# Optimization experiments

Hardware: AMD Instinct MI355X
Metric: run time of the kernel (lower is better)

The kernel has to match this reference:

```python
import jax, jax.numpy as jnp
import numpy as np

V, T, E, H, L, B = 50257, 1024, 1024, 16, 12, 4
HD = E // H
FF = 4 * E
EPS = 1e-5


def layer_norm(x, g, b):
    m = jnp.mean(x, axis=-1, keepdims=True)
    v = jnp.mean((x - m) ** 2, axis=-1, keepdims=True)
    return (x - m) * jax.lax.rsqrt(v + EPS) * g + b


def setup_inputs() -> dict:
    key = jax.random.key(0)
    ks = jax.random.split(key, 24)
    s = 0.02
    inp = {
        'idx': jax.random.randint(ks[0], (B, T), 0, V),
        'targets': jax.random.randint(ks[1], (B, T), 0, V),
        'tok_emb': jax.random.normal(ks[2], (V, E), jnp.float32) * s,
        'pos_emb': jax.random.normal(ks[3], (T, E), jnp.float32) * s,
        'Wq': jax.random.normal(ks[4], (L, E, H, HD), jnp.float32) * s,
        'Wk': jax.random.normal(ks[5], (L, E, H, HD), jnp.float32) * s,
        'Wv': jax.random.normal(ks[6], (L, E, H, HD), jnp.float32) * s,
        'Wo': jax.random.normal(ks[7], (L, E, E), jnp.float32) * s,
        'bo': jnp.zeros((L, E), jnp.float32),
        'ln1_g': jnp.ones((L, E), jnp.float32),
        'ln1_b': jnp.zeros((L, E), jnp.float32),
        'ln2_g': jnp.ones((L, E), jnp.float32),
        'ln2_b': jnp.zeros((L, E), jnp.float32),
        'W1': jax.random.normal(ks[8], (L, E, FF), jnp.float32) * s,
        'b1': jnp.zeros((L, FF), jnp.float32),
        'W2': jax.random.normal(ks[9], (L, FF, E), jnp.float32) * s,
        'b2': jnp.zeros((L, E), jnp.float32),
        'lnf_g': jnp.ones((E,), jnp.float32),
        'lnf_b': jnp.zeros((E,), jnp.float32),
        'Whead': jax.random.normal(ks[10], (E, V), jnp.float32) * s,
        'bhead': jnp.zeros((V,), jnp.float32),
    }
    return inp


def forward(idx, targets, tok_emb, pos_emb, Wq, Wk, Wv, Wo, bo, ln1_g, ln1_b,
            ln2_g, ln2_b, W1, b1, W2, b2, lnf_g, lnf_b, Whead, bhead):
    Bc, Tc = idx.shape
    x = tok_emb[idx] + pos_emb[:Tc]  # [B,T,E]
    scale = HD ** -0.5
    causal = jnp.tril(jnp.ones((Tc, Tc), bool))
    for l in range(L):
        h = layer_norm(x, ln1_g[l], ln1_b[l])
        q = jnp.einsum('bte,ehd->bthd', h, Wq[l])
        k = jnp.einsum('bte,ehd->bthd', h, Wk[l])
        v = jnp.einsum('bte,ehd->bthd', h, Wv[l])
        wei = jnp.einsum('bqhd,bkhd->bhqk', q, k) * scale
        wei = jnp.where(causal, wei, -jnp.inf)
        wei = jax.nn.softmax(wei, axis=-1)
        att = jnp.einsum('bhqk,bkhd->bqhd', wei, v).reshape(Bc, Tc, E)
        x = x + att @ Wo[l] + bo[l]
        h = layer_norm(x, ln2_g[l], ln2_b[l])
        # torch nn.GELU default is exact (erf) gelu
        ff = jax.nn.gelu(h @ W1[l] + b1[l], approximate=False) @ W2[l] + b2[l]
        x = x + ff
    x = layer_norm(x, lnf_g, lnf_b)
    logits = x @ Whead + bhead  # [B,T,V]
    logp = jax.nn.log_softmax(logits, axis=-1)
    nll = -jnp.take_along_axis(logp, targets[..., None], axis=-1)[..., 0]
    loss = jnp.mean(nll)
    return logits, loss


def reference(idx, targets, tok_emb, pos_emb, Wq, Wk, Wv, Wo, bo, ln1_g, ln1_b,
              ln2_g, ln2_b, W1, b1, W2, b2, lnf_g, lnf_b, Whead, bhead):
    return forward(idx, targets, tok_emb, pos_emb, Wq, Wk, Wv, Wo, bo, ln1_g,
                   ln1_b, ln2_g, ln2_b, W1, b1, W2, b2, lnf_g, lnf_b, Whead, bhead)
```

## Files before the change

### kernel.cpp

```cpp
#include <hip/hip_runtime.h>
#include <cstdint>
#include <cstddef>

typedef unsigned short u16;
typedef __bf16 bf16x8 __attribute__((ext_vector_type(8)));
typedef float f32x4 __attribute__((ext_vector_type(4)));
typedef unsigned short u16x8 __attribute__((ext_vector_type(8)));
typedef unsigned short u16x4 __attribute__((ext_vector_type(4)));

constexpr int cV  = 50257;
constexpr int cVp = 50432;
constexpr int cNT = cVp / 256;
constexpr int cT  = 1024;
constexpr int cE  = 1024;
constexpr int cL  = 12;
constexpr int cFF = 4096;
constexpr int cBT = 4096;

__device__ __forceinline__ u16 f2bf(float f) {
  union { float f; unsigned u; } x; x.f = f;
  unsigned r = x.u + 0x7fffu + ((x.u >> 16) & 1u);
  return (u16)(r >> 16);
}

__device__ __forceinline__ void gload16(const void* g, void* l) {
  __builtin_amdgcn_global_load_lds(
      (const __attribute__((address_space(1))) void*)g,
      (__attribute__((address_space(3))) void*)l, 16, 0, 0);
}

__device__ __forceinline__ int swzoff(int row, int chunk) {
  return ((chunk ^ (row & 7) ^ ((row >> 3) & 7)) << 4);
}

__device__ __forceinline__ int xcd_swz(int id, int nwg) {
  if ((nwg & 7) == 0) { const int q = nwg >> 3; return (id & 7) * q + (id >> 3); }
  return id;
}

__global__ __launch_bounds__(256) void k_embed(const int* __restrict__ idx,
    const float* __restrict__ tok, const float* __restrict__ pos,
    float* __restrict__ x) {
  const int row = blockIdx.x;
  const int t = row & (cT - 1);
  const int tk = idx[row];
  const float4* tv = (const float4*)(tok + (size_t)tk * cE);
  const float4* pv = (const float4*)(pos + (size_t)t * cE);
  float4* xv = (float4*)(x + (size_t)row * cE);
  const int i = threadIdx.x;
  float4 a = tv[i];
  float4 p = pv[i];
  a.x += p.x; a.y += p.y; a.z += p.z; a.w += p.w;
  xv[i] = a;
}

__global__ __launch_bounds__(256) void k_ln(const float* __restrict__ x,
    const float* __restrict__ gw, const float* __restrict__ bw,
    u16* __restrict__ out) {
  const int row = blockIdx.x;
  const int t = threadIdx.x;
  const float4 v = ((const float4*)(x + (size_t)row * cE))[t];
  float s1 = v.x + v.y + v.z + v.w;
  float s2 = v.x * v.x + v.y * v.y + v.z * v.z + v.w * v.w;
  #pragma unroll
  for (int off = 32; off; off >>= 1) {
    s1 += __shfl_xor(s1, off);
    s2 += __shfl_xor(s2, off);
  }
  __shared__ float red[8];
  const int wid = t >> 6;
  if ((t & 63) == 0) { red[wid] = s1; red[4 + wid] = s2; }
  __syncthreads();
  s1 = red[0] + red[1] + red[2] + red[3];
  s2 = red[4] + red[5] + red[6] + red[7];
  const float mean = s1 * (1.0f / cE);
  const float var = s2 * (1.0f / cE) - mean * mean;
  const float rs = rsqrtf(var + 1e-5f);
  const float4 g4 = ((const float4*)gw)[t];
  const float4 b4 = ((const float4*)bw)[t];
  u16x4 o;
  o[0] = f2bf((v.x - mean) * rs * g4.x + b4.x);
  o[1] = f2bf((v.y - mean) * rs * g4.y + b4.y);
  o[2] = f2bf((v.z - mean) * rs * g4.z + b4.z);
  o[3] = f2bf((v.w - mean) * rs * g4.w + b4.w);
  *(u16x4*)(out + (size_t)row * cE + t * 4) = o;
}

__global__ __launch_bounds__(256) void k_cvt_t(const float* __restrict__ src,
    u16* __restrict__ dst, int K, int Nsrc, size_t sstride, size_t dstride) {
  __shared__ float tile[32][33];
  const float* s = src + blockIdx.z * sstride;
  u16* d = dst + blockIdx.z * dstride;
  const int n0 = blockIdx.x * 32, k0 = blockIdx.y * 32;
  const int t = threadIdx.x;
  const int c = t & 31, r0 = t >> 5;
  #pragma unroll
  for (int i = 0; i < 4; ++i) {
    const int kl = r0 + i * 8;
    const int n = n0 + c;
    tile[kl][c] = (n < Nsrc) ? s[(size_t)(k0 + kl) * Nsrc + n] : 0.0f;
  }
  __syncthreads();
  #pragma unroll
  for (int i = 0; i < 4; ++i) {
    const int nl = r0 + i * 8;
    d[(size_t)(n0 + nl) * K + k0 + c] = f2bf(tile[c][nl]);
  }
}

template<int EPI>
__global__ __launch_bounds__(512, 4) void k_gemm2(
    const u16* __restrict__ A, const u16* __restrict__ Bt,
    const float* __restrict__ bias, u16* __restrict__ obf,
    float* __restrict__ of, int K, int Nout, int ntile, int mt,
    float* __restrict__ pm, float* __restrict__ ps) {
  __shared__ __align__(16) char smem[49152];
  const int tid = threadIdx.x;
  const int lane = tid & 63;
  const int wid = tid >> 6;
  const int wg = (int)blockIdx.x;
  const int bm = wg % mt;
  const int bn = wg / mt;
  const int wm = wid >> 2, wn = wid & 3;
  const int l15 = lane & 15, lg = lane >> 4;

  f32x4 acc[4][4];
  #pragma unroll
  for (int i = 0; i < 4; ++i)
    #pragma unroll
    for (int j = 0; j < 4; ++j) { f32x4 z = {0.f,0.f,0.f,0.f}; acc[i][j] = z; }

  const u16* Ab = A + (size_t)(bm * 128) * K;
  const u16* Bb = Bt + (size_t)(bn * 256) * K;
  const int nt = K >> 5;

  auto stage = [&](int t) {
    char* buf = smem + ((t & 1) ? 24576 : 0);
    const int kt = t << 5;
    {
      const int r = tid >> 2, c = tid & 3;
      gload16(Ab + (size_t)r * K + kt + ((c ^ ((r >> 1) & 3)) << 3),
              buf + tid * 16);
    }
    #pragma unroll
    for (int p = 0; p < 2; ++p) {
      const int L = p * 512 + tid;
      const int r = L >> 2, c = L & 3;
      gload16(Bb + (size_t)r * K + kt + ((c ^ ((r >> 1) & 3)) << 3),
              buf + 8192 + L * 16);
    }
  };

  stage(0);
  for (int t = 0; t < nt; ++t) {
    __syncthreads();
    if (t + 1 < nt) stage(t + 1);
    char* cs = smem + ((t & 1) ? 24576 : 0);
    const char* csB = cs + 8192;
    bf16x8 af[4], bfr[4];
    #pragma unroll
    for (int mi = 0; mi < 4; ++mi) {
      const int row = wm * 64 + mi * 16 + l15;
      af[mi] = *(const bf16x8*)(cs + row * 64 + ((lg ^ ((row >> 1) & 3)) << 4));
    }
    #pragma unroll
    for (int ni = 0; ni < 4; ++ni) {
      const int row = wn * 64 + ni * 16 + l15;
      bfr[ni] = *(const bf16x8*)(csB + row * 64 + ((lg ^ ((row >> 1) & 3)) << 4));
    }
    #pragma unroll
    for (int ni = 0; ni < 4; ++ni)
      #pragma unroll
      for (int mi = 0; mi < 4; ++mi)
        acc[mi][ni] = __builtin_amdgcn_mfma_f32_16x16x32_bf16(af[mi], bfr[ni], acc[mi][ni], 0, 0, 0);
  }

  if constexpr (EPI == 3) {
    __syncthreads();
    float* pb = (float*)smem;
    #pragma unroll
    for (int mi = 0; mi < 4; ++mi) {
      const int grow = bm * 128 + wm * 64 + mi * 16 + lg * 4;
      float rm[4];
      #pragma unroll
      for (int r = 0; r < 4; ++r) rm[r] = -1e30f;
      #pragma unroll
      for (int ni = 0; ni < 4; ++ni) {
        const int gcol = bn * 256 + wn * 64 + ni * 16 + l15;
        const bool ok = gcol < Nout;
        const float bb = ok ? bias[gcol] : 0.0f;
        #pragma unroll
        for (int r = 0; r < 4; ++r) {
          const float v = ok ? (acc[mi][ni][r] + bb) : -1e30f;
          acc[mi][ni][r] = v;
          if (ok) of[(size_t)(grow + r) * Nout + gcol] = v;
          rm[r] = fmaxf(rm[r], v);
        }
      }
      #pragma unroll
      for (int r = 0; r < 4; ++r) {
        float m = rm[r];
        #pragma unroll
        for (int off = 1; off < 16; off <<= 1) m = fmaxf(m, __shfl_xor(m, off));
        float s = 0.f;
        #pragma unroll
        for (int ni = 0; ni < 4; ++ni) s += __expf(acc[mi][ni][r] - m);
        #pragma unroll
        for (int off = 1; off < 16; off <<= 1) s += __shfl_xor(s, off);
        if (l15 == 0) {
          const int lrow = wm * 64 + mi * 16 + lg * 4 + r;
          pb[(lrow * 4 + wn) * 2] = m;
          pb[(lrow * 4 + wn) * 2 + 1] = s;
        }
      }
    }
    __syncthreads();
    if (tid < 128) {
      float m = -1e30f, s = 0.f;
      #pragma unroll
      for (int q = 0; q < 4; ++q) {
        const float m2 = pb[(tid * 4 + q) * 2];
        const float s2 = pb[(tid * 4 + q) * 2 + 1];
        const float M = fmaxf(m, m2);
        s = s * __expf(m - M) + s2 * __expf(m2 - M);
        m = M;
      }
      const size_t grow = (size_t)(bm * 128 + tid);
      pm[grow * ntile + bn] = m;
      ps[grow * ntile + bn] = s;
    }
  } else {
    #pragma unroll
    for (int mi = 0; mi < 4; ++mi) {
      const int grow = bm * 128 + wm * 64 + mi * 16 + lg * 4;
      #pragma unroll
      for (int ni = 0; ni < 4; ++ni) {
        const int gcol = bn * 256 + wn * 64 + ni * 16 + l15;
        #pragma unroll
        for (int r = 0; r < 4; ++r) {
          const float a = acc[mi][ni][r];
          if constexpr (EPI == 0) {
            obf[(size_t)(gcol >> 10) * 4194304 + (size_t)(grow + r) * 1024 + (gcol & 1023)] = f2bf(a);
          } else {
            const float gv = a + bias[gcol];
            obf[(size_t)(grow + r) * Nout + gcol] = f2bf(0.5f * gv * (1.0f + erff(gv * 0.70710678118f)));
          }
        }
      }
    }
  }
}

__global__ __launch_bounds__(256) void k_gemm_s(
    const u16* __restrict__ A, const u16* __restrict__ Bt,
    const float* __restrict__ bias, float* __restrict__ of,
    int K, int Nout, int mt) {
  __shared__ __align__(16) char smem[49152];
  const int tid = threadIdx.x;
  const int lane = tid & 63;
  const int wid = tid >> 6;
  const int wg = xcd_swz((int)blockIdx.x, (int)gridDim.x);
  const int bm = wg % mt;
  const int bn = wg / mt;
  const int wr = wid >> 1, wc = wid & 1;
  const int l15 = lane & 15, lg = lane >> 4;

  f32x4 acc[2][4];
  #pragma unroll
  for (int i = 0; i < 2; ++i)
    #pragma unroll
    for (int j = 0; j < 4; ++j) { f32x4 z = {0.f,0.f,0.f,0.f}; acc[i][j] = z; }

  const u16* Ab = A + (size_t)(bm * 64) * K;
  const u16* Bb = Bt + (size_t)(bn * 128) * K;
  const int nt = K >> 6;

  auto stage = [&](int t, char* buf) {
    const int kt = (t < nt ? t : nt - 1) << 6;
    #pragma unroll
    for (int p = 0; p < 2; ++p) {
      const int L = p * 256 + tid;
      const int row = L >> 3, cc = L & 7;
      gload16(Ab + (size_t)row * K + kt + ((cc ^ (row & 7)) << 3), buf + L * 16);
    }
    #pragma unroll
    for (int p = 0; p < 4; ++p) {
      const int L = p * 256 + tid;
      const int row = L >> 3, cc = L & 7;
      gload16(Bb + (size_t)row * K + kt + ((cc ^ (row & 7)) << 3), buf + 8192 + L * 16);
    }
  };
  stage(0, smem);
  stage(1, smem + 24576);

  for (int t = 0; t < nt; ++t) {
    char* cs = smem + ((t & 1) ? 24576 : 0);
    const char* csB = cs + 8192;
    asm volatile("s_waitcnt vmcnt(6)" ::: "memory");
    __builtin_amdgcn_s_barrier();

    bf16x8 af[2][2], bfr[4][2];
    #pragma unroll
    for (int mi = 0; mi < 2; ++mi) {
      const int row = wr * 32 + mi * 16 + l15;
      #pragma unroll
      for (int kk = 0; kk < 2; ++kk)
        af[mi][kk] = *(const bf16x8*)(cs + row * 128 + (((kk * 4 + lg) ^ (row & 7)) << 4));
    }
    #pragma unroll
    for (int ni = 0; ni < 4; ++ni) {
      const int row = wc * 64 + ni * 16 + l15;
      #pragma unroll
      for (int kk = 0; kk < 2; ++kk)
        bfr[ni][kk] = *(const bf16x8*)(csB + row * 128 + (((kk * 4 + lg) ^ (row & 7)) << 4));
    }
    __builtin_amdgcn_sched_barrier(0);
    __builtin_amdgcn_s_setprio(1);
    #pragma unroll
    for (int ni = 0; ni < 4; ++ni)
      #pragma unroll
      for (int mi = 0; mi < 2; ++mi)
        acc[mi][ni] = __builtin_amdgcn_mfma_f32_16x16x32_bf16(af[mi][0], bfr[ni][0], acc[mi][ni], 0, 0, 0);
    __builtin_amdgcn_s_setprio(0);
    __builtin_amdgcn_sched_barrier(0);
    asm volatile("s_waitcnt lgkmcnt(0)" ::: "memory");
    __builtin_amdgcn_sched_barrier(0);
    __builtin_amdgcn_s_barrier();

    stage(t + 2, cs);
    __builtin_amdgcn_sched_barrier(0);
    __builtin_amdgcn_s_setprio(1);
    #pragma unroll
    for (int ni = 0; ni < 4; ++ni)
      #pragma unroll
      for (int mi = 0; mi < 2; ++mi)
        acc[mi][ni] = __builtin_amdgcn_mfma_f32_16x16x32_bf16(af[mi][1], bfr[ni][1], acc[mi][ni], 0, 0, 0);
    __builtin_amdgcn_s_setprio(0);
    __builtin_amdgcn_sched_barrier(0);
  }
  asm volatile("s_waitcnt vmcnt(0)" ::: "memory");

  #pragma unroll
  for (int mi = 0; mi < 2; ++mi) {
    const int grow = bm * 64 + wr * 32 + mi * 16 + lg * 4;
    #pragma unroll
    for (int ni = 0; ni < 4; ++ni) {
      const int gcol = bn * 128 + wc * 64 + ni * 16 + l15;
      #pragma unroll
      for (int r = 0; r < 4; ++r)
        of[(size_t)(grow + r) * Nout + gcol] += acc[mi][ni][r] + bias[gcol];
    }
  }
}

__global__ __launch_bounds__(256) void k_gemm_legacy3(
    const u16* __restrict__ A, const float* __restrict__ B0,
    const float* __restrict__ bias, float* __restrict__ of,
    int M, int N, int K) {
  __shared__ u16 Al[128 * 32];
  __shared__ u16 Bl[32 * 128];
  const int tid = threadIdx.x;
  const int lane = tid & 63;
  const int wid = tid >> 6;
  const int bn = blockIdx.x;
  const int bm = blockIdx.y;
  const int wr = wid >> 1, wc = wid & 1;
  const int l15 = lane & 15, lg = lane >> 4;
  f32x4 acc[4][4];
  #pragma unroll
  for (int i = 0; i < 4; ++i)
    #pragma unroll
    for (int j = 0; j < 4; ++j) { f32x4 z = {0.f,0.f,0.f,0.f}; acc[i][j] = z; }
  const u16* Abase = A + (size_t)(bm * 128) * K;
  const int ar0 = tid >> 2;
  const int ac0 = (tid & 3) * 8;
  const int brow = tid >> 3;
  const int bc0 = (tid & 7) * 16;
  for (int kt = 0; kt < K; kt += 32) {
    *(u16x8*)(Al + ar0 * 32 + ac0) =
        *(const u16x8*)(Abase + (size_t)ar0 * K + kt + ac0);
    *(u16x8*)(Al + (ar0 + 64) * 32 + ac0) =
        *(const u16x8*)(Abase + (size_t)(ar0 + 64) * K + kt + ac0);
    {
      const float* bsrc = B0 + (size_t)(kt + brow) * N + bn * 128 + bc0;
      alignas(16) u16 tmp[16];
      const int colbase = bn * 128 + bc0;
      #pragma unroll
      for (int q = 0; q < 16; ++q)
        tmp[q] = f2bf((colbase + q < N) ? bsrc[q] : 0.0f);
      *(u16x8*)(Bl + brow * 128 + bc0) = *(const u16x8*)tmp;
      *(u16x8*)(Bl + brow * 128 + bc0 + 8) = *(const u16x8*)(tmp + 8);
    }
    __syncthreads();
    bf16x8 af[4];
    #pragma unroll
    for (int mi = 0; mi < 4; ++mi)
      af[mi] = *(const bf16x8*)(Al + (wr * 64 + mi * 16 + l15) * 32 + lg * 8);
    #pragma unroll
    for (int ni = 0; ni < 4; ++ni) {
      u16x8 tv;
      #pragma unroll
      for (int i = 0; i < 8; ++i)
        tv[i] = Bl[(lg * 8 + i) * 128 + wc * 64 + ni * 16 + l15];
      const bf16x8 bfr = __builtin_bit_cast(bf16x8, tv);
      #pragma unroll
      for (int mi = 0; mi < 4; ++mi)
        acc[mi][ni] = __builtin_amdgcn_mfma_f32_16x16x32_bf16(af[mi], bfr, acc[mi][ni], 0, 0, 0);
    }
    __syncthreads();
  }
  #pragma unroll
  for (int mi = 0; mi < 4; ++mi) {
    const int grow = bm * 128 + wr * 64 + mi * 16 + lg * 4;
    #pragma unroll
    for (int ni = 0; ni < 4; ++ni) {
      const int gcol = bn * 128 + wc * 64 + ni * 16 + l15;
      #pragma unroll
      for (int r = 0; r < 4; ++r)
        if (gcol < N) of[(size_t)(grow + r) * N + gcol] = acc[mi][ni][r] + bias[gcol];
    }
  }
}

__global__ __launch_bounds__(256, 2) void k_attn(
    const u16* __restrict__ qg, const u16* __restrict__ kg,
    const u16* __restrict__ vg, u16* __restrict__ og) {
  __shared__ u16 Kl[64 * 64];
  __shared__ u16 Vt[64 * 64];
  __shared__ u16 Pl[4][16 * 64];
  const int tid = threadIdx.x;
  const int lane = tid & 63;
  const int w = tid >> 6;
  const int qt = blockIdx.x;
  const int bh = blockIdx.y;
  const int b = bh >> 4, h = bh & 15;
  const int l15 = lane & 15, lg = lane >> 4;
  char* KlB = (char*)Kl;
  char* VtB = (char*)Vt;
  char* PlB = (char*)(Pl[w]);

  const size_t qrow0 = (size_t)b * cT + qt * 64 + w * 16;
  bf16x8 aq[2];
  #pragma unroll
  for (int c = 0; c < 2; ++c)
    aq[c] = *(const bf16x8*)(qg + (qrow0 + l15) * cE + h * 64 + c * 32 + lg * 8);

  f32x4 acco[4];
  #pragma unroll
  for (int j = 0; j < 4; ++j) { f32x4 z = {0.f,0.f,0.f,0.f}; acco[j] = z; }
  float mrun[4], lrun[4];
  #pragma unroll
  for (int r = 0; r < 4; ++r) { mrun[r] = -1e30f; lrun[r] = 0.f; }

  for (int kt = 0; kt <= qt; ++kt) {
    const size_t krow0 = (size_t)b * cT + kt * 64;
    #pragma unroll
    for (int u = 0; u < 2; ++u) {
      const int un = tid + u * 256;
      const int rr = un >> 3, c8 = (un & 7) * 8;
      *(u16x8*)(KlB + rr * 128 + swzoff(rr, c8 >> 3)) =
          *(const u16x8*)(kg + (krow0 + rr) * cE + h * 64 + c8);
      const u16x8 vv = *(const u16x8*)(vg + (krow0 + rr) * cE + h * 64 + c8);
      #pragma unroll
      for (int i = 0; i < 8; ++i)
        *(u16*)(VtB + (c8 + i) * 128 + swzoff(c8 + i, rr >> 3) + (rr & 7) * 2) = vv[i];
    }
    __syncthreads();

    f32x4 s[4];
    #pragma unroll
    for (int j = 0; j < 4; ++j) { f32x4 z = {0.f,0.f,0.f,0.f}; s[j] = z; }
    #pragma unroll
    for (int c = 0; c < 2; ++c) {
      #pragma unroll
      for (int j = 0; j < 4; ++j) {
        const int n = j * 16 + l15;
        const bf16x8 kb2 = *(const bf16x8*)(KlB + n * 128 + swzoff(n, c * 4 + lg));
        s[j] = __builtin_amdgcn_mfma_f32_16x16x32_bf16(aq[c], kb2, s[j], 0, 0, 0);
      }
    }

    float sv[4][4];
    const bool diag = (kt == qt);
    #pragma unroll
    for (int j = 0; j < 4; ++j)
      #pragma unroll
      for (int r = 0; r < 4; ++r) {
        float xs = s[j][r] * 0.125f;
        if (diag && (j * 16 + l15) > (w * 16 + lg * 4 + r)) xs = -1e30f;
        sv[j][r] = xs;
      }

    float corr[4];
    #pragma unroll
    for (int r = 0; r < 4; ++r) {
      float mx = fmaxf(fmaxf(sv[0][r], sv[1][r]), fmaxf(sv[2][r], sv[3][r]));
      #pragma unroll
      for (int off = 1; off < 16; off <<= 1) mx = fmaxf(mx, __shfl_xor(mx, off));
      const float mnew = fmaxf(mrun[r], mx);
      corr[r] = __expf(mrun[r] - mnew);
      float rs = 0.f;
      #pragma unroll
      for (int j = 0; j < 4; ++j) {
        const float p = __expf(sv[j][r] - mnew);
        sv[j][r] = p;
        rs += p;
      }
      #pragma unroll
      for (int off = 1; off < 16; off <<= 1) rs += __shfl_xor(rs, off);
      lrun[r] = lrun[r] * corr[r] + rs;
      mrun[r] = mnew;
    }

    #pragma unroll
    for (int j = 0; j < 4; ++j)
      #pragma unroll
      for (int r = 0; r < 4; ++r) {
        const int qr = lg * 4 + r, kc = j * 16 + l15;
        *(u16*)(PlB + qr * 128 + swzoff(qr, kc >> 3) + (kc & 7) * 2) = f2bf(sv[j][r]);
        acco[j][r] *= corr[r];
      }

    #pragma unroll
    for (int c = 0; c < 2; ++c) {
      const bf16x8 pa = *(const bf16x8*)(PlB + l15 * 128 + swzoff(l15, c * 4 + lg));
      #pragma unroll
      for (int j = 0; j < 4; ++j) {
        const int n = j * 16 + l15;
        const bf16x8 vb2 = *(const bf16x8*)(VtB + n * 128 + swzoff(n, c * 4 + lg));
        acco[j] = __builtin_amdgcn_mfma_f32_16x16x32_bf16(pa, vb2, acco[j], 0, 0, 0);
      }
    }
    __syncthreads();
  }

  #pragma unroll
  for (int j = 0; j < 4; ++j)
    #pragma unroll
    for (int r = 0; r < 4; ++r)
      og[(qrow0 + lg * 4 + r) * cE + h * 64 + j * 16 + l15] = f2bf(acco[j][r] / lrun[r]);
}

__global__ __launch_bounds__(256) void k_nll2(const float* __restrict__ pm,
    const float* __restrict__ ps, const float* __restrict__ logits,
    const int* __restrict__ tgt, float* __restrict__ nll, int NT) {
  const int row = blockIdx.x * 4 + (threadIdx.x >> 6);
  const int lane = threadIdx.x & 63;
  float m = -1e30f, s = 0.f;
  for (int i = lane; i < NT; i += 64) {
    const float m2 = pm[(size_t)row * NT + i];
    const float s2 = ps[(size_t)row * NT + i];
    const float M = fmaxf(m, m2);
    s = s * __expf(m - M) + s2 * __expf(m2 - M);
    m = M;
  }
  #pragma unroll
  for (int off = 1; off < 64; off <<= 1) {
    const float m2 = __shfl_xor(m, off);
    const float s2 = __shfl_xor(s, off);
    const float M = fmaxf(m, m2);
    s = s * __expf(m - M) + s2 * __expf(m2 - M);
    m = M;
  }
  if (lane == 0)
    nll[row] = logf(s) + m - logits[(size_t)row * cV + tgt[row]];
}

__global__ __launch_bounds__(256) void k_nll(const float* __restrict__ logits,
    const int* __restrict__ tgt, float* __restrict__ nll) {
  const int row = blockIdx.x;
  const float* lp = logits + (size_t)row * cV;
  const int t = threadIdx.x;
  __shared__ float red[8];
  const int wid = t >> 6, lane = t & 63;
  float mx = -1e30f;
  for (int i = t; i < cV; i += 256) mx = fmaxf(mx, lp[i]);
  #pragma unroll
  for (int off = 32; off; off >>= 1) mx = fmaxf(mx, __shfl_xor(mx, off));
  if (lane == 0) red[wid] = mx;
  __syncthreads();
  mx = fmaxf(fmaxf(red[0], red[1]), fmaxf(red[2], red[3]));
  float s = 0.f;
  for (int i = t; i < cV; i += 256) s += __expf(lp[i] - mx);
  #pragma unroll
  for (int off = 32; off; off >>= 1) s += __shfl_xor(s, off);
  if (lane == 0) red[4 + wid] = s;
  __syncthreads();
  if (t == 0) {
    s = red[4] + red[5] + red[6] + red[7];
    nll[row] = logf(s) + mx - lp[tgt[row]];
  }
}

__global__ __launch_bounds__(256) void k_loss(const float* __restrict__ nll,
    float* __restrict__ out) {
  const int t = threadIdx.x;
  float s = 0.f;
  for (int i = t; i < cBT; i += 256) s += nll[i];
  #pragma unroll
  for (int off = 32; off; off >>= 1) s += __shfl_xor(s, off);
  __shared__ float red[4];
  if ((t & 63) == 0) red[t >> 6] = s;
  __syncthreads();
  if (t == 0) out[0] = (red[0] + red[1] + red[2] + red[3]) * (1.0f / cBT);
}

extern "C" void kernel_launch(void* const* d_in, const int* in_sizes, int n_in,
                              void* d_out, int out_size, void* d_ws, size_t ws_size,
                              hipStream_t stream) {
  const int*   idx  = (const int*)d_in[0];
  const int*   tgt  = (const int*)d_in[1];
  const float* tok  = (const float*)d_in[2];
  const float* pos  = (const float*)d_in[3];
  const float* Wq   = (const float*)d_in[4];
  const float* Wk   = (const float*)d_in[5];
  const float* Wv   = (const float*)d_in[6];
  const float* Wo   = (const float*)d_in[7];
  const float* bo   = (const float*)d_in[8];
  const float* ln1g = (const float*)d_in[9];
  const float* ln1b = (const float*)d_in[10];
  const float* ln2g = (const float*)d_in[11];
  const float* ln2b = (const float*)d_in[12];
  const float* W1   = (const float*)d_in[13];
  const float* b1   = (const float*)d_in[14];
  const float* W2   = (const float*)d_in[15];
  const float* b2   = (const float*)d_in[16];
  const float* lnfg = (const float*)d_in[17];
  const float* lnfb = (const float*)d_in[18];
  const float* Wh   = (const float*)d_in[19];
  const float* bh   = (const float*)d_in[20];

  char* ob = (char*)d_out;
  float* x    = (float*)ob;
  u16* hb     = (u16*)(ob + (16u << 20));
  u16* qb     = (u16*)(ob + (24u << 20));
  u16* kb     = (u16*)(ob + (32u << 20));
  u16* vb     = (u16*)(ob + (40u << 20));
  u16* abuf   = (u16*)(ob + (48u << 20));
  u16* fbuf   = (u16*)(ob + (56u << 20));
  u16* W3T    = (u16*)(ob + (128u << 20));
  u16* WoT    = (u16*)(ob + (200u << 20));
  u16* W1T    = (u16*)(ob + (224u << 20));
  u16* W2T    = (u16*)(ob + (320u << 20));
  u16* hf     = (u16*)d_ws;
  float* nll  = (float*)((char*)d_ws + 8388608);
  u16* WheadT = (u16*)((char*)d_ws + 8404992);
  const size_t whead_end = 8404992u + (size_t)cVp * cE * 2u;
  float* pmax = (float*)((char*)d_ws + whead_end);
  float* psum = (float*)((char*)d_ws + whead_end + (size_t)cBT * cNT * 4);
  const size_t ws_need = whead_end + 2u * (size_t)cBT * cNT * 4;
  const bool fast_head = ws_size >= ws_need;

  float* logits = (float*)d_out;
  float* loss = logits + (size_t)cBT * cV;

  const dim3 blk(256);
  const size_t e2 = (size_t)cE * cE, ef = (size_t)cE * cFF;

  k_cvt_t<<<dim3(32, 32, cL), blk, 0, stream>>>(Wq, W3T,          cE, cE, e2, 3 * e2);
  k_cvt_t<<<dim3(32, 32, cL), blk, 0, stream>>>(Wk, W3T + e2,     cE, cE, e2, 3 * e2);
  k_cvt_t<<<dim3(32, 32, cL), blk, 0, stream>>>(Wv, W3T + 2 * e2, cE, cE, e2, 3 * e2);
  k_cvt_t<<<dim3(32, 32, cL), blk, 0, stream>>>(Wo, WoT, cE, cE, e2, e2);
  k_cvt_t<<<dim3(128, 32, cL), blk, 0, stream>>>(W1, W1T, cE, cFF, ef, ef);
  k_cvt_t<<<dim3(32, 128, cL), blk, 0, stream>>>(W2, W2T, cFF, cE, ef, ef);
  if (fast_head)
    k_cvt_t<<<dim3(cVp / 32, 32, 1), blk, 0, stream>>>(Wh, WheadT, cE, cV, 0, 0);

  k_embed<<<dim3(cBT), blk, 0, stream>>>(idx, tok, pos, x);
  for (int l = 0; l < cL; ++l) {
    k_ln<<<dim3(cBT), blk, 0, stream>>>(x, ln1g + l * cE, ln1b + l * cE, hb);
    k_gemm2<0><<<dim3(32 * 12), dim3(512), 0, stream>>>(hb, W3T + l * 3 * e2,
        nullptr, qb, nullptr, cE, 3072, 0, 32, nullptr, nullptr);
    k_attn<<<dim3(16, 64), blk, 0, stream>>>(qb, kb, vb, abuf);
    k_gemm_s<<<dim3(512), blk, 0, stream>>>(abuf, WoT + l * e2, bo + l * cE, x, cE, cE, 64);
    k_ln<<<dim3(cBT), blk, 0, stream>>>(x, ln2g + l * cE, ln2b + l * cE, hb);
    k_gemm2<2><<<dim3(32 * 16), dim3(512), 0, stream>>>(hb, W1T + l * ef,
        b1 + l * cFF, fbuf, nullptr, cE, cFF, 0, 32, nullptr, nullptr);
    k_gemm_s<<<dim3(512), blk, 0, stream>>>(fbuf, W2T + l * ef, b2 + l * cE, x, cFF, cE, 64);
  }
  k_ln<<<dim3(cBT), blk, 0, stream>>>(x, lnfg, lnfb, hf);
  if (fast_head) {
    k_gemm2<3><<<dim3(32 * cNT), dim3(512), 0, stream>>>(hf, WheadT, bh,
        nullptr, logits, cE, cV, cNT, 32, pmax, psum);
    k_nll2<<<dim3(cBT / 4), blk, 0, stream>>>(pmax, psum, logits, tgt, nll, cNT);
  } else {
    k_gemm_legacy3<<<dim3(393, 32), blk, 0, stream>>>(hf, Wh, bh, logits, cBT, cV, cE);
    k_nll<<<dim3(cBT), blk, 0, stream>>>(logits, tgt, nll);
  }
  k_loss<<<dim3(1), blk, 0, stream>>>(nll, loss);
}
```

Measured before the change: 4.371 ms.

## Share K/V tiles across 128 query rows in attention and widen weight-transpose tiles

The attention kernel now runs 512 threads per block covering 128 query rows, so each loaded K/V tile feeds eight warps instead of four, halving the K/V global reloads. Warps whose query rows lie before the current key tile skip the compute but still take part in the loads and barriers. The weight transpose-convert kernel uses 64-wide tiles with float4 loads and 4-element bf16 stores to cut memory transactions. The risks are idle warps on the last key tile of each block and fewer attention blocks in flight.

```diff
diff --git a/kernel.cpp b/kernel.cpp
--- a/kernel.cpp
+++ b/kernel.cpp
@@ -88,23 +88,37 @@
 
 __global__ __launch_bounds__(256) void k_cvt_t(const float* __restrict__ src,
     u16* __restrict__ dst, int K, int Nsrc, size_t sstride, size_t dstride) {
-  __shared__ float tile[32][33];
+  __shared__ float tile[32][65];
   const float* s = src + blockIdx.z * sstride;
   u16* d = dst + blockIdx.z * dstride;
-  const int n0 = blockIdx.x * 32, k0 = blockIdx.y * 32;
+  const int n0 = blockIdx.x * 64, k0 = blockIdx.y * 32;
   const int t = threadIdx.x;
-  const int c = t & 31, r0 = t >> 5;
-  #pragma unroll
-  for (int i = 0; i < 4; ++i) {
-    const int kl = r0 + i * 8;
-    const int n = n0 + c;
-    tile[kl][c] = (n < Nsrc) ? s[(size_t)(k0 + kl) * Nsrc + n] : 0.0f;
+  #pragma unroll
+  for (int p = 0; p < 2; ++p) {
+    const int li = p * 256 + t;
+    const int k = li >> 4;
+    const int n4 = (li & 15) * 4;
+    const float* sp = s + (size_t)(k0 + k) * Nsrc + n0 + n4;
+    if ((n0 + n4 + 3 < Nsrc) && ((((size_t)(k0 + k) * Nsrc + n0 + n4) & 3) == 0)) {
+      const float4 f = *(const float4*)sp;
+      tile[k][n4] = f.x; tile[k][n4 + 1] = f.y;
+      tile[k][n4 + 2] = f.z; tile[k][n4 + 3] = f.w;
+    } else {
+      #pragma unroll
+      for (int i = 0; i < 4; ++i)
+        tile[k][n4 + i] = (n0 + n4 + i < Nsrc) ? sp[i] : 0.0f;
+    }
   }
   __syncthreads();
   #pragma unroll
-  for (int i = 0; i < 4; ++i) {
-    const int nl = r0 + i * 8;
-    d[(size_t)(n0 + nl) * K + k0 + c] = f2bf(tile[c][nl]);
+  for (int p = 0; p < 2; ++p) {
+    const int si = p * 256 + t;
+    const int n = si >> 3;
+    const int k4 = (si & 7) * 4;
+    u16x4 o;
+    #pragma unroll
+    for (int i = 0; i < 4; ++i) o[i] = f2bf(tile[k4 + i][n]);
+    *(u16x4*)(d + (size_t)(n0 + n) * K + k0 + k4) = o;
   }
 }
 
@@ -422,16 +436,16 @@
   }
 }
 
-__global__ __launch_bounds__(256, 2) void k_attn(
+__global__ __launch_bounds__(512, 2) void k_attn(
     const u16* __restrict__ qg, const u16* __restrict__ kg,
     const u16* __restrict__ vg, u16* __restrict__ og) {
   __shared__ u16 Kl[64 * 64];
   __shared__ u16 Vt[64 * 64];
-  __shared__ u16 Pl[4][16 * 64];
+  __shared__ u16 Pl[8][16 * 64];
   const int tid = threadIdx.x;
   const int lane = tid & 63;
   const int w = tid >> 6;
-  const int qt = blockIdx.x;
+  const int bx = blockIdx.x;
   const int bh = blockIdx.y;
   const int b = bh >> 4, h = bh & 15;
   const int l15 = lane & 15, lg = lane >> 4;
@@ -439,7 +453,9 @@
   char* VtB = (char*)Vt;
   char* PlB = (char*)(Pl[w]);
 
-  const size_t qrow0 = (size_t)b * cT + qt * 64 + w * 16;
+  const int qwr = bx * 128 + w * 16;
+  const int diagkt = qwr >> 6;
+  const size_t qrow0 = (size_t)b * cT + qwr;
   bf16x8 aq[2];
   #pragma unroll
   for (int c = 0; c < 2; ++c)
@@ -452,12 +468,11 @@
   #pragma unroll
   for (int r = 0; r < 4; ++r) { mrun[r] = -1e30f; lrun[r] = 0.f; }
 
-  for (int kt = 0; kt <= qt; ++kt) {
+  const int ktmax = 2 * bx + 1;
+  for (int kt = 0; kt <= ktmax; ++kt) {
     const size_t krow0 = (size_t)b * cT + kt * 64;
-    #pragma unroll
-    for (int u = 0; u < 2; ++u) {
-      const int un = tid + u * 256;
-      const int rr = un >> 3, c8 = (un & 7) * 8;
+    {
+      const int rr = tid >> 3, c8 = (tid & 7) * 8;
       *(u16x8*)(KlB + rr * 128 + swzoff(rr, c8 >> 3)) =
           *(const u16x8*)(kg + (krow0 + rr) * cE + h * 64 + c8);
       const u16x8 vv = *(const u16x8*)(vg + (krow0 + rr) * cE + h * 64 + c8);
@@ -467,68 +482,70 @@
     }
     __syncthreads();
 
-    f32x4 s[4];
-    #pragma unroll
-    for (int j = 0; j < 4; ++j) { f32x4 z = {0.f,0.f,0.f,0.f}; s[j] = z; }
-    #pragma unroll
-    for (int c = 0; c < 2; ++c) {
-      #pragma unroll
-      for (int j = 0; j < 4; ++j) {
-        const int n = j * 16 + l15;
-        const bf16x8 kb2 = *(const bf16x8*)(KlB + n * 128 + swzoff(n, c * 4 + lg));
-        s[j] = __builtin_amdgcn_mfma_f32_16x16x32_bf16(aq[c], kb2, s[j], 0, 0, 0);
+    if (kt <= diagkt) {
+      f32x4 s[4];
+      #pragma unroll
+      for (int j = 0; j < 4; ++j) { f32x4 z = {0.f,0.f,0.f,0.f}; s[j] = z; }
+      #pragma unroll
+      for (int c = 0; c < 2; ++c) {
+        #pragma unroll
+        for (int j = 0; j < 4; ++j) {
+          const int n = j * 16 + l15;
+          const bf16x8 kb2 = *(const bf16x8*)(KlB + n * 128 + swzoff(n, c * 4 + lg));
+          s[j] = __builtin_amdgcn_mfma_f32_16x16x32_bf16(aq[c], kb2, s[j], 0, 0, 0);
+        }
       }
-    }
-
-    float sv[4][4];
-    const bool diag = (kt == qt);
-    #pragma unroll
-    for (int j = 0; j < 4; ++j)
+
+      float sv[4][4];
+      const bool diag = (kt == diagkt);
+      #pragma unroll
+      for (int j = 0; j < 4; ++j)
+        #pragma unroll
+        for (int r = 0; r < 4; ++r) {
+          float xs = s[j][r] * 0.125f;
+          if (diag && (kt * 64 + j * 16 + l15) > (qwr + lg * 4 + r)) xs = -1e30f;
+          sv[j][r] = xs;
+        }
+
+      float corr[4];
       #pragma unroll
       for (int r = 0; r < 4; ++r) {
-        float xs = s[j][r] * 0.125f;
-        if (diag && (j * 16 + l15) > (w * 16 + lg * 4 + r)) xs = -1e30f;
-        sv[j][r] = xs;
+        float mx = fmaxf(fmaxf(sv[0][r], sv[1][r]), fmaxf(sv[2][r], sv[3][r]));
+        #pragma unroll
+        for (int off = 1; off < 16; off <<= 1) mx = fmaxf(mx, __shfl_xor(mx, off));
+        const float mnew = fmaxf(mrun[r], mx);
+        corr[r] = __expf(mrun[r] - mnew);
+        float rs = 0.f;
+        #pragma unroll
+        for (int j = 0; j < 4; ++j) {
+          const float p = __expf(sv[j][r] - mnew);
+          sv[j][r] = p;
+          rs += p;
+        }
+        #pragma unroll
+        for (int off = 1; off < 16; off <<= 1) rs += __shfl_xor(rs, off);
+        lrun[r] = lrun[r] * corr[r] + rs;
+        mrun[r] = mnew;
       }
 
-    float corr[4];
-    #pragma unroll
-    for (int r = 0; r < 4; ++r) {
-      float mx = fmaxf(fmaxf(sv[0][r], sv[1][r]), fmaxf(sv[2][r], sv[3][r]));
-      #pragma unroll
-      for (int off = 1; off < 16; off <<= 1) mx = fmaxf(mx, __shfl_xor(mx, off));
-      const float mnew = fmaxf(mrun[r], mx);
-      corr[r] = __expf(mrun[r] - mnew);
-      float rs = 0.f;
-      #pragma unroll
-      for (int j = 0; j < 4; ++j) {
-        const float p = __expf(sv[j][r] - mnew);
-        sv[j][r] = p;
-        rs += p;
-      }
-      #pragma unroll
-      for (int off = 1; off < 16; off <<= 1) rs += __shfl_xor(rs, off);
-      lrun[r] = lrun[r] * corr[r] + rs;
-      mrun[r] = mnew;
-    }
-
-    #pragma unroll
-    for (int j = 0; j < 4; ++j)
-      #pragma unroll
-      for (int r = 0; r < 4; ++r) {
-        const int qr = lg * 4 + r, kc = j * 16 + l15;
-        *(u16*)(PlB + qr * 128 + swzoff(qr, kc >> 3) + (kc & 7) * 2) = f2bf(sv[j][r]);
-        acco[j][r] *= corr[r];
-      }
-
-    #pragma unroll
-    for (int c = 0; c < 2; ++c) {
-      const bf16x8 pa = *(const bf16x8*)(PlB + l15 * 128 + swzoff(l15, c * 4 + lg));
-      #pragma unroll
-      for (int j = 0; j < 4; ++j) {
-        const int n = j * 16 + l15;
-        const bf16x8 vb2 = *(const bf16x8*)(VtB + n * 128 + swzoff(n, c * 4 + lg));
-        acco[j] = __builtin_amdgcn_mfma_f32_16x16x32_bf16(pa, vb2, acco[j], 0, 0, 0);
+      #pragma unroll
+      for (int j = 0; j < 4; ++j)
+        #pragma unroll
+        for (int r = 0; r < 4; ++r) {
+          const int qr = lg * 4 + r, kc = j * 16 + l15;
+          *(u16*)(PlB + qr * 128 + swzoff(qr, kc >> 3) + (kc & 7) * 2) = f2bf(sv[j][r]);
+          acco[j][r] *= corr[r];
+        }
+
+      #pragma unroll
+      for (int c = 0; c < 2; ++c) {
+        const bf16x8 pa = *(const bf16x8*)(PlB + l15 * 128 + swzoff(l15, c * 4 + lg));
+        #pragma unroll
+        for (int j = 0; j < 4; ++j) {
+          const int n = j * 16 + l15;
+          const bf16x8 vb2 = *(const bf16x8*)(VtB + n * 128 + swzoff(n, c * 4 + lg));
+          acco[j] = __builtin_amdgcn_mfma_f32_16x16x32_bf16(pa, vb2, acco[j], 0, 0, 0);
+        }
       }
     }
     __syncthreads();
@@ -657,21 +674,21 @@
   const dim3 blk(256);
   const size_t e2 = (size_t)cE * cE, ef = (size_t)cE * cFF;
 
-  k_cvt_t<<<dim3(32, 32, cL), blk, 0, stream>>>(Wq, W3T,          cE, cE, e2, 3 * e2);
-  k_cvt_t<<<dim3(32, 32, cL), blk, 0, stream>>>(Wk, W3T + e2,     cE, cE, e2, 3 * e2);
-  k_cvt_t<<<dim3(32, 32, cL), blk, 0, stream>>>(Wv, W3T + 2 * e2, cE, cE, e2, 3 * e2);
-  k_cvt_t<<<dim3(32, 32, cL), blk, 0, stream>>>(Wo, WoT, cE, cE, e2, e2);
-  k_cvt_t<<<dim3(128, 32, cL), blk, 0, stream>>>(W1, W1T, cE, cFF, ef, ef);
-  k_cvt_t<<<dim3(32, 128, cL), blk, 0, stream>>>(W2, W2T, cFF, cE, ef, ef);
+  k_cvt_t<<<dim3(16, 32, cL), blk, 0, stream>>>(Wq, W3T,          cE, cE, e2, 3 * e2);
+  k_cvt_t<<<dim3(16, 32, cL), blk, 0, stream>>>(Wk, W3T + e2,     cE, cE, e2, 3 * e2);
+  k_cvt_t<<<dim3(16, 32, cL), blk, 0, stream>>>(Wv, W3T + 2 * e2, cE, cE, e2, 3 * e2);
+  k_cvt_t<<<dim3(16, 32, cL), blk, 0, stream>>>(Wo, WoT, cE, cE, e2, e2);
+  k_cvt_t<<<dim3(64, 32, cL), blk, 0, stream>>>(W1, W1T, cE, cFF, ef, ef);
+  k_cvt_t<<<dim3(16, 128, cL), blk, 0, stream>>>(W2, W2T, cFF, cE, ef, ef);
   if (fast_head)
-    k_cvt_t<<<dim3(cVp / 32, 32, 1), blk, 0, stream>>>(Wh, WheadT, cE, cV, 0, 0);
+    k_cvt_t<<<dim3(cVp / 64, 32, 1), blk, 0, stream>>>(Wh, WheadT, cE, cV, 0, 0);
 
   k_embed<<<dim3(cBT), blk, 0, stream>>>(idx, tok, pos, x);
   for (int l = 0; l < cL; ++l) {
     k_ln<<<dim3(cBT), blk, 0, stream>>>(x, ln1g + l * cE, ln1b + l * cE, hb);
     k_gemm2<0><<<dim3(32 * 12), dim3(512), 0, stream>>>(hb, W3T + l * 3 * e2,
         nullptr, qb, nullptr, cE, 3072, 0, 32, nullptr, nullptr);
-    k_attn<<<dim3(16, 64), blk, 0, stream>>>(qb, kb, vb, abuf);
+    k_attn<<<dim3(8, 64), dim3(512), 0, stream>>>(qb, kb, vb, abuf);
     k_gemm_s<<<dim3(512), blk, 0, stream>>>(abuf, WoT + l * e2, bo + l * cE, x, cE, cE, 64);
     k_ln<<<dim3(cBT), blk, 0, stream>>>(x, ln2g + l * cE, ln2b + l * cE, hb);
     k_gemm2<2><<<dim3(32 * 16), dim3(512), 0, stream>>>(hb, W1T + l * ef,
```

Result: faster. 4.108 ms (-6.0%).
